# Kernel tuning notes

Hardware: AMD Instinct MI355X
Metric: run time of the kernel (lower is better)

Reference implementation:

```python
import jax, jax.numpy as jnp
import numpy as np

D_LATENT = 8
N_CENTERS = 48
CHANNELS = 64
PM_STEPS = 4
DT, BETA, CLAMP = 0.12, 1.0, 3.0
SIGMA_E, SIGMA_I, K_E, K_I, GAIN = 0.6, 1.2, 0.8, 1.0, 0.06


def setup_inputs() -> dict:
    key = jax.random.key(0)
    ks = jax.random.split(key, 12)
    B = 8192
    x = jax.random.normal(ks[0], (B, 784), dtype=jnp.float32)
    # encoder params (torch Linear default-ish init scale)
    W1 = jax.random.normal(ks[1], (784, 256), dtype=jnp.float32) * (1.0 / np.sqrt(784))
    b1 = jnp.zeros((256,), jnp.float32)
    W2 = jax.random.normal(ks[2], (256, D_LATENT), dtype=jnp.float32) * (1.0 / np.sqrt(256))
    b2 = jnp.zeros((D_LATENT,), jnp.float32)
    centers = jax.random.normal(ks[3], (N_CENTERS, D_LATENT), dtype=jnp.float32) * 0.7
    mus = jnp.ones((N_CENTERS,), jnp.float32) * 0.4
    projW = jax.random.normal(ks[4], (D_LATENT, CHANNELS), dtype=jnp.float32) * (1.0 / np.sqrt(D_LATENT))
    projb = jnp.zeros((CHANNELS,), jnp.float32)
    roW = jax.random.normal(ks[5], (CHANNELS, 10), dtype=jnp.float32) * (1.0 / np.sqrt(CHANNELS))
    rob = jnp.zeros((10,), jnp.float32)
    return {"x": x, "W1": W1, "b1": b1, "W2": W2, "b2": b2,
            "centers": centers, "mus": mus, "projW": projW, "projb": projb,
            "roW": roW, "rob": rob, "T": 5}


def _pm_field(z, centers, mus):
    # one PMField forward: `PM_STEPS` gradient-flow steps on z [B, d]
    for _ in range(PM_STEPS):
        diff = z[:, None, :] - centers[None, :, :]            # [B, C, d]
        r2 = jnp.sum(diff * diff, axis=-1) + 1e-4              # [B, C]
        r = jnp.sqrt(r2)
        n = 1.0 + jnp.sum(mus[None, :] / r, axis=1)            # [B]
        g = -jnp.sum(mus[None, :, None] * diff / (r * r2)[:, :, None], axis=1)  # [B, d]
        z = z + DT * BETA * (g / n[:, None])
        z = jnp.clip(z, -CLAMP, CLAMP)
    return z


def _lateral_ei(z, h):
    # kernel computed with no_grad in torch -> stop_gradient here
    sq = jnp.sum(z * z, axis=1)                                # [B]
    dist2 = jnp.maximum(sq[:, None] + sq[None, :] - 2.0 * (z @ z.T), 0.0)
    Ke = K_E * jnp.exp(-dist2 / (2.0 * SIGMA_E ** 2))
    Ki = K_I * jnp.exp(-dist2 / (2.0 * SIGMA_I ** 2))
    K = Ke - Ki
    K = K / (jnp.sum(K, axis=1, keepdims=True) + 1e-6)
    K = jax.lax.stop_gradient(K)
    return GAIN * (K @ h)


def reference(x, W1, b1, W2, b2, centers, mus, projW, projb, roW, rob, T):
    z = jnp.tanh(x @ W1 + b1) @ W2 + b2                        # encoder -> [B, d]
    h = jnp.zeros((x.shape[0], CHANNELS), x.dtype)
    logits = None
    for _ in range(T):
        z = _pm_field(z, centers, mus)
        h = 0.9 * h + 0.1 * jnp.tanh(z @ projW + projb)
        h = h + _lateral_ei(z, h)
        logits = h @ roW + rob
    return logits, z, h
```

## Files before the change

kernel.cpp:

```cpp
#include <hip/hip_runtime.h>
#include <hip/hip_bf16.h>
#include <math.h>

#define B_N      8192
#define IN_DIM   784
#define HID      256
#define DL       8
#define NC       48
#define CH       64
#define NCLS     10
#define T_ITERS  5
#define TILES    128

#define DT_      0.12f
#define CLAMP_   3.0f
#define GAIN_    0.06f
#define SQIL2    0.70776814f
#define ONE_BF16 0x3F80u

#if defined(__has_builtin)
#if __has_builtin(__builtin_amdgcn_exp2f)
#define EXP2(x) __builtin_amdgcn_exp2f(x)
#endif
#endif
#ifndef EXP2
#define EXP2(x) exp2f(x)
#endif

typedef __attribute__((ext_vector_type(8))) short short8v;
typedef __attribute__((ext_vector_type(4))) float f32x4;

__device__ __forceinline__ unsigned int pack_bf16_rhu(float lo, float hi) {
    unsigned int b0 = __builtin_bit_cast(unsigned int, lo);
    unsigned int b1 = __builtin_bit_cast(unsigned int, hi);
    return ((b0 + 0x8000u) >> 16) | ((b1 + 0x8000u) & 0xFFFF0000u);
}
__device__ __forceinline__ unsigned short bf16_1(float x) {
    return (unsigned short)((__builtin_bit_cast(unsigned int, x) + 0x8000u) >> 16);
}
__device__ __forceinline__ float bf16_to_f(unsigned short h) {
    return __builtin_bit_cast(float, ((unsigned int)h) << 16);
}

__device__ __forceinline__ void z_split(const float4 a, const float4 b,
                                        uint4& Whi, uint4& Wlo, unsigned int& Wc)
{
    float u[8] = {SQIL2*a.x, SQIL2*a.y, SQIL2*a.z, SQIL2*a.w,
                  SQIL2*b.x, SQIL2*b.y, SQIL2*b.z, SQIL2*b.w};
    float sq = 0.f;
    #pragma unroll
    for (int d = 0; d < 8; ++d) sq = fmaf(u[d], u[d], sq);
    float cn = -0.5f * sq;
    unsigned short hi[8]; float lo[8];
    #pragma unroll
    for (int d = 0; d < 8; ++d) {
        hi[d] = bf16_1(u[d]);
        lo[d] = u[d] - bf16_to_f(hi[d]);
    }
    unsigned short ch_ = bf16_1(cn);
    unsigned short cl_ = bf16_1(cn - bf16_to_f(ch_));
    Whi.x = (unsigned int)hi[0] | ((unsigned int)hi[1] << 16);
    Whi.y = (unsigned int)hi[2] | ((unsigned int)hi[3] << 16);
    Whi.z = (unsigned int)hi[4] | ((unsigned int)hi[5] << 16);
    Whi.w = (unsigned int)hi[6] | ((unsigned int)hi[7] << 16);
    Wlo.x = pack_bf16_rhu(lo[0], lo[1]); Wlo.y = pack_bf16_rhu(lo[2], lo[3]);
    Wlo.z = pack_bf16_rhu(lo[4], lo[5]); Wlo.w = pack_bf16_rhu(lo[6], lo[7]);
    Wc = (unsigned int)ch_ | ((unsigned int)cl_ << 16);
}

__global__ __launch_bounds__(256) void k_gemm1_tanh(
    const float* __restrict__ x, const float* __restrict__ W1,
    const float* __restrict__ b1, float* __restrict__ H1)
{
    __shared__ float As[16][36];
    __shared__ float Bs[16][64];
    const int tid = threadIdx.x;
    const int row0 = blockIdx.x * 32;
    const int col0 = blockIdx.y * 64;
    const int tr = tid >> 4, tc = tid & 15;
    float acc[2][4] = {};
    for (int k0 = 0; k0 < IN_DIM; k0 += 16) {
        if (tid < 128) {
            int m = tid >> 2, kq = tid & 3;
            float4 v = *(const float4*)(x + (size_t)(row0 + m) * IN_DIM + k0 + kq * 4);
            As[kq*4+0][m] = v.x; As[kq*4+1][m] = v.y;
            As[kq*4+2][m] = v.z; As[kq*4+3][m] = v.w;
        }
        {
            int kk = tid >> 4, n4 = tid & 15;
            *(float4*)(&Bs[kk][n4*4]) =
                *(const float4*)(W1 + (size_t)(k0 + kk) * HID + col0 + n4 * 4);
        }
        __syncthreads();
        #pragma unroll
        for (int kk = 0; kk < 16; ++kk) {
            float a0 = As[kk][tr*2];
            float a1 = As[kk][tr*2+1];
            float4 b = *(const float4*)(&Bs[kk][tc*4]);
            acc[0][0] += a0*b.x; acc[0][1] += a0*b.y;
            acc[0][2] += a0*b.z; acc[0][3] += a0*b.w;
            acc[1][0] += a1*b.x; acc[1][1] += a1*b.y;
            acc[1][2] += a1*b.z; acc[1][3] += a1*b.w;
        }
        __syncthreads();
    }
    #pragma unroll
    for (int i = 0; i < 2; ++i) {
        int r = row0 + tr*2 + i;
        #pragma unroll
        for (int j = 0; j < 4; ++j) {
            int c = col0 + tc*4 + j;
            H1[(size_t)r * HID + c] = tanhf(acc[i][j] + b1[c]);
        }
    }
}

__global__ __launch_bounds__(256) void k_gemm2(
    const float* __restrict__ H1, const float* __restrict__ W2,
    const float* __restrict__ b2, float* __restrict__ zbuf)
{
    __shared__ float W2s[HID][DL];
    const int tid = threadIdx.x;
    for (int l = tid; l < HID * DL; l += 256) W2s[l >> 3][l & 7] = W2[l];
    __syncthreads();
    const int row = blockIdx.x * 32 + (tid >> 3);
    const int d = tid & 7;
    float acc = b2[d];
    const float* hr = H1 + (size_t)row * HID;
    for (int k = 0; k < HID; k += 4) {
        float4 hv = *(const float4*)(hr + k);
        acc += hv.x * W2s[k][d] + hv.y * W2s[k+1][d]
             + hv.z * W2s[k+2][d] + hv.w * W2s[k+3][d];
    }
    zbuf[(size_t)row * DL + d] = acc;
}

template<int S, bool HP>
__global__ __launch_bounds__(256) void k_pm_proj(
    const float* __restrict__ centers, const float* __restrict__ mus,
    const float* __restrict__ projW, const float* __restrict__ projb,
    float* __restrict__ zbuf, float* __restrict__ hB,
    unsigned short* __restrict__ hTb,
    const float* __restrict__ pAcc, const float* __restrict__ pDen)
{
    __shared__ float4 cs4[NC][2];
    __shared__ float mu_s[NC];
    __shared__ float pW[DL][CH];
    __shared__ float pb[CH];
    const int tid = threadIdx.x;
    for (int l = tid; l < NC * 2; l += 256) cs4[l >> 1][l & 1] = ((const float4*)centers)[l];
    if (tid < NC) mu_s[tid] = mus[tid];
    for (int l = tid; l < DL * CH; l += 256) pW[l >> 6][l & 63] = projW[l];
    if (tid < CH) pb[tid] = projb[tid];
    __syncthreads();

    const int rloc = tid >> 3;
    const int dl = tid & 7;
    const int row = blockIdx.x * 32 + rloc;

    float4 cza[6], czb[6];
    float mur[6];
    #pragma unroll
    for (int k = 0; k < 6; ++k) {
        cza[k] = cs4[dl + 8*k][0];
        czb[k] = cs4[dl + 8*k][1];
        mur[k] = mu_s[dl + 8*k];
    }

    float z[8];
    {
        const float4* zp = (const float4*)(zbuf + (size_t)row * DL);
        float4 a = zp[0], b = zp[1];
        z[0]=a.x; z[1]=a.y; z[2]=a.z; z[3]=a.w;
        z[4]=b.x; z[5]=b.y; z[6]=b.z; z[7]=b.w;
    }

    #pragma unroll
    for (int step = 0; step < 4; ++step) {
        float np = 0.f;
        float gp[8] = {0,0,0,0,0,0,0,0};
        #pragma unroll
        for (int k = 0; k < 6; ++k) {
            float d0 = z[0]-cza[k].x, d1 = z[1]-cza[k].y;
            float d2 = z[2]-cza[k].z, d3 = z[3]-cza[k].w;
            float d4 = z[4]-czb[k].x, d5 = z[5]-czb[k].y;
            float d6 = z[6]-czb[k].z, d7 = z[7]-czb[k].w;
            float r2 = 1e-4f;
            r2 = fmaf(d0,d0,r2); r2 = fmaf(d1,d1,r2);
            r2 = fmaf(d2,d2,r2); r2 = fmaf(d3,d3,r2);
            r2 = fmaf(d4,d4,r2); r2 = fmaf(d5,d5,r2);
            r2 = fmaf(d6,d6,r2); r2 = fmaf(d7,d7,r2);
            float r = sqrtf(r2);
            float mr = mur[k] / r;
            np += mr;
            float t = mr / r2;
            gp[0] = fmaf(-t, d0, gp[0]); gp[1] = fmaf(-t, d1, gp[1]);
            gp[2] = fmaf(-t, d2, gp[2]); gp[3] = fmaf(-t, d3, gp[3]);
            gp[4] = fmaf(-t, d4, gp[4]); gp[5] = fmaf(-t, d5, gp[5]);
            gp[6] = fmaf(-t, d6, gp[6]); gp[7] = fmaf(-t, d7, gp[7]);
        }
        #pragma unroll
        for (int m = 1; m < 8; m <<= 1) {
            np += __shfl_xor(np, m);
            #pragma unroll
            for (int d = 0; d < 8; ++d) gp[d] += __shfl_xor(gp[d], m);
        }
        float s = DT_ / (1.f + np);
        #pragma unroll
        for (int d = 0; d < 8; ++d) {
            z[d] = fmaf(s, gp[d], z[d]);
            z[d] = fminf(fmaxf(z[d], -CLAMP_), CLAMP_);
        }
    }

    {
        float zout = z[0];
        #pragma unroll
        for (int d = 1; d < 8; ++d) zout = (dl == d) ? z[d] : zout;
        zbuf[(size_t)row * DL + dl] = zout;
    }

    const int c0 = dl * 8;
    float hin[8];
    if (HP) {
        float den = 1e-6f;
        #pragma unroll
        for (int s = 0; s < S; ++s) den += pDen[s * B_N + row];
        float inv = GAIN_ / den;
        #pragma unroll
        for (int q = 0; q < 2; ++q) {
            float4 a = {0.f, 0.f, 0.f, 0.f};
            #pragma unroll
            for (int s = 0; s < S; ++s) {
                float4 p = *(const float4*)(pAcc + (size_t)s * B_N * CH
                                            + (size_t)row * CH + c0 + q * 4);
                a.x += p.x; a.y += p.y; a.z += p.z; a.w += p.w;
            }
            float4 hm = *(const float4*)(hB + (size_t)row * CH + c0 + q * 4);
            hin[q*4+0] = fmaf(inv, a.x, hm.x);
            hin[q*4+1] = fmaf(inv, a.y, hm.y);
            hin[q*4+2] = fmaf(inv, a.z, hm.z);
            hin[q*4+3] = fmaf(inv, a.w, hm.w);
        }
    } else {
        #pragma unroll
        for (int k = 0; k < 8; ++k) hin[k] = 0.f;
    }
    #pragma unroll
    for (int k = 0; k < 8; ++k) {
        int c = c0 + k;
        float s = pb[c];
        #pragma unroll
        for (int dd = 0; dd < DL; ++dd) s = fmaf(z[dd], pW[dd][c], s);
        hin[k] = 0.9f * hin[k] + 0.1f * tanhf(s);
    }
    float4 o0 = {hin[0], hin[1], hin[2], hin[3]};
    float4 o1 = {hin[4], hin[5], hin[6], hin[7]};
    *(float4*)(hB + (size_t)row * CH + c0)     = o0;
    *(float4*)(hB + (size_t)row * CH + c0 + 4) = o1;

    {
        const int jl = row & 63;
        const int colp = (jl & 35) | ((jl & 12) << 1) | ((jl & 16) >> 2);
        const size_t tb = (size_t)(row & ~63) + colp;
        #pragma unroll
        for (int k = 0; k < 8; ++k)
            hTb[(size_t)(c0 + k) * B_N + tb] = bf16_1(hin[k]);
    }
}

template<int S>
__global__ __launch_bounds__(128, 2) void k_lateral(
    const float* __restrict__ zbuf, const unsigned short* __restrict__ hTb,
    float* __restrict__ pAcc, float* __restrict__ pDen)
{
    __shared__ __align__(16) unsigned short zA[2][64 * 24];
    __shared__ __align__(16) unsigned short hsT[2][CH][72];
    const int tid  = threadIdx.x;
    const int lane = tid & 63;
    const int wv   = tid >> 6;
    const int l15  = lane & 15;
    const int g    = lane >> 4;
    const int rowbase = blockIdx.x * 64;
    const int t0 = (TILES * blockIdx.y) / S;
    const int t1 = (TILES * (blockIdx.y + 1)) / S;
    const int chS = tid >> 1, hfS = tid & 1;

    short8v bZa, bZb;
    #pragma unroll
    for (int setb = 0; setb < 2; ++setb) {
        const int irow = rowbase + 32 * wv + 16 * setb + l15;
        const float4* zp = (const float4*)(zbuf + (size_t)irow * DL);
        uint4 Whi, Wlo; unsigned int Wc;
        z_split(zp[0], zp[1], Whi, Wlo, Wc);
        union { unsigned int u[4]; short8v v; } uh, ul, ua;
        uh.u[0]=Whi.x; uh.u[1]=Whi.y; uh.u[2]=Whi.z; uh.u[3]=Whi.w;
        ul.u[0]=Wlo.x; ul.u[1]=Wlo.y; ul.u[2]=Wlo.z; ul.u[3]=Wlo.w;
        ua.u[0] = ONE_BF16 | (ONE_BF16 << 16);
        ua.u[1] = Wc; ua.u[2] = 0; ua.u[3] = 0;
        short8v bz = (g == 2) ? ul.v : ((g == 3) ? ua.v : uh.v);
        if (setb == 0) bZa = bz; else bZb = bz;
    }
    const int offsh = (g == 1) ? 8 : ((g == 3) ? 16 : 0);

    short8v bones;
    {
        union { unsigned int u[4]; short8v v; } uo;
        uo.u[0] = uo.u[1] = uo.u[2] = uo.u[3] = ONE_BF16 | (ONE_BF16 << 16);
        bones = uo.v;
    }

    f32x4 accA0 = {0,0,0,0}, accA1 = {0,0,0,0}, accA2 = {0,0,0,0}, accA3 = {0,0,0,0};
    f32x4 accB0 = {0,0,0,0}, accB1 = {0,0,0,0}, accB2 = {0,0,0,0}, accB3 = {0,0,0,0};
    f32x4 acc4A = {0,0,0,0}, acc4B = {0,0,0,0};
    const f32x4 zc = {0,0,0,0};

    {
        const int jb = t0 * 64;
        if (tid < 64) {
            const float4* zp = (const float4*)(zbuf + (size_t)(jb + tid) * DL);
            uint4 Whi, Wlo; unsigned int Wc;
            z_split(zp[0], zp[1], Whi, Wlo, Wc);
            uint4 W2v; W2v.x = Wc; W2v.y = ONE_BF16 | (ONE_BF16 << 16);
            W2v.z = 0; W2v.w = 0;
            unsigned short* dst = &zA[0][tid * 24];
            *(uint4*)(dst)      = Whi;
            *(uint4*)(dst + 8)  = Wlo;
            *(uint4*)(dst + 16) = W2v;
        }
        const unsigned short* hs = hTb + (size_t)chS * B_N + jb + hfS * 32;
        *(uint4*)(&hsT[0][chS][hfS*32])      = *(const uint4*)(hs);
        *(uint4*)(&hsT[0][chS][hfS*32 + 8])  = *(const uint4*)(hs + 8);
        *(uint4*)(&hsT[0][chS][hfS*32 + 16]) = *(const uint4*)(hs + 16);
        *(uint4*)(&hsT[0][chS][hfS*32 + 24]) = *(const uint4*)(hs + 24);
    }

    #pragma unroll 1
    for (int jt = t0; jt < t1; ++jt) {
        const int cur = (jt - t0) & 1;
        const bool more = (jt + 1 < t1);
        uint4 h0n, h1n, h2n, h3n;
        float4 zna, znb;
        if (more) {
            const int jb2 = (jt + 1) * 64;
            const unsigned short* hs = hTb + (size_t)chS * B_N + jb2 + hfS * 32;
            h0n = *(const uint4*)(hs);
            h1n = *(const uint4*)(hs + 8);
            h2n = *(const uint4*)(hs + 16);
            h3n = *(const uint4*)(hs + 24);
            if (tid < 64) {
                const float4* zp = (const float4*)(zbuf + (size_t)(jb2 + tid) * DL);
                zna = zp[0]; znb = zp[1];
            }
        }
        __syncthreads();

        f32x4 gacA[4], gacB[4];
        #pragma unroll
        for (int t = 0; t < 4; ++t) {
            short8v az = *(const short8v*)(&zA[cur][(t * 16 + l15) * 24 + offsh]);
            gacA[t] = __builtin_amdgcn_mfma_f32_16x16x32_bf16(az, bZa, zc, 0, 0, 0);
            gacB[t] = __builtin_amdgcn_mfma_f32_16x16x32_bf16(az, bZb, zc, 0, 0, 0);
        }

        short8v afrA[2], afrB[2];
        #pragma unroll
        for (int kb = 0; kb < 2; ++kb) {
            float w8[8];
            #pragma unroll
            for (int m = 0; m < 8; ++m) {
                float out = gacA[2 * kb + (m >> 2)][m & 3];
                float e1 = EXP2(out);
                float e2 = e1 * e1;
                float e4 = e2 * e2;
                float e8 = e4 * e4;
                w8[m] = fmaf(0.8f, e8, -e2);
            }
            union { unsigned int u[4]; short8v v; } uf;
            uf.u[0] = pack_bf16_rhu(w8[0], w8[1]);
            uf.u[1] = pack_bf16_rhu(w8[2], w8[3]);
            uf.u[2] = pack_bf16_rhu(w8[4], w8[5]);
            uf.u[3] = pack_bf16_rhu(w8[6], w8[7]);
            afrA[kb] = uf.v;
        }
        #pragma unroll
        for (int kb = 0; kb < 2; ++kb) {
            float w8[8];
            #pragma unroll
            for (int m = 0; m < 8; ++m) {
                float out = gacB[2 * kb + (m >> 2)][m & 3];
                float e1 = EXP2(out);
                float e2 = e1 * e1;
                float e4 = e2 * e2;
                float e8 = e4 * e4;
                w8[m] = fmaf(0.8f, e8, -e2);
            }
            union { unsigned int u[4]; short8v v; } uf;
            uf.u[0] = pack_bf16_rhu(w8[0], w8[1]);
            uf.u[1] = pack_bf16_rhu(w8[2], w8[3]);
            uf.u[2] = pack_bf16_rhu(w8[4], w8[5]);
            uf.u[3] = pack_bf16_rhu(w8[6], w8[7]);
            afrB[kb] = uf.v;
        }

        #pragma unroll
        for (int kb = 0; kb < 2; ++kb) {
            const int jo = kb * 32 + g * 8;
            short8v b0 = *(const short8v*)&hsT[cur][ 0 + l15][jo];
            short8v b1 = *(const short8v*)&hsT[cur][16 + l15][jo];
            short8v b2 = *(const short8v*)&hsT[cur][32 + l15][jo];
            short8v b3 = *(const short8v*)&hsT[cur][48 + l15][jo];
            accA0 = __builtin_amdgcn_mfma_f32_16x16x32_bf16(afrA[kb], b0, accA0, 0, 0, 0);
            accA1 = __builtin_amdgcn_mfma_f32_16x16x32_bf16(afrA[kb], b1, accA1, 0, 0, 0);
            accA2 = __builtin_amdgcn_mfma_f32_16x16x32_bf16(afrA[kb], b2, accA2, 0, 0, 0);
            accA3 = __builtin_amdgcn_mfma_f32_16x16x32_bf16(afrA[kb], b3, accA3, 0, 0, 0);
            accB0 = __builtin_amdgcn_mfma_f32_16x16x32_bf16(afrB[kb], b0, accB0, 0, 0, 0);
            accB1 = __builtin_amdgcn_mfma_f32_16x16x32_bf16(afrB[kb], b1, accB1, 0, 0, 0);
            accB2 = __builtin_amdgcn_mfma_f32_16x16x32_bf16(afrB[kb], b2, accB2, 0, 0, 0);
            accB3 = __builtin_amdgcn_mfma_f32_16x16x32_bf16(afrB[kb], b3, accB3, 0, 0, 0);
            acc4A = __builtin_amdgcn_mfma_f32_16x16x32_bf16(afrA[kb], bones, acc4A, 0, 0, 0);
            acc4B = __builtin_amdgcn_mfma_f32_16x16x32_bf16(afrB[kb], bones, acc4B, 0, 0, 0);
        }
        __syncthreads();

        if (more) {
            const int nb = cur ^ 1;
            if (tid < 64) {
                uint4 Whi, Wlo; unsigned int Wc;
                z_split(zna, znb, Whi, Wlo, Wc);
                uint4 W2v; W2v.x = Wc; W2v.y = ONE_BF16 | (ONE_BF16 << 16);
                W2v.z = 0; W2v.w = 0;
                unsigned short* dst = &zA[nb][tid * 24];
                *(uint4*)(dst)      = Whi;
                *(uint4*)(dst + 8)  = Wlo;
                *(uint4*)(dst + 16) = W2v;
            }
            *(uint4*)(&hsT[nb][chS][hfS*32])      = h0n;
            *(uint4*)(&hsT[nb][chS][hfS*32 + 8])  = h1n;
            *(uint4*)(&hsT[nb][chS][hfS*32 + 16]) = h2n;
            *(uint4*)(&hsT[nb][chS][hfS*32 + 24]) = h3n;
        }
    }

    float* pA = pAcc + (size_t)blockIdx.y * (B_N * CH) + (size_t)rowbase * CH;
    #pragma unroll
    for (int r = 0; r < 4; ++r) {
        int giA = 32 * wv + g * 4 + r;
        int giB = giA + 16;
        pA[(size_t)giA * CH +  0 + l15] = accA0[r];
        pA[(size_t)giA * CH + 16 + l15] = accA1[r];
        pA[(size_t)giA * CH + 32 + l15] = accA2[r];
        pA[(size_t)giA * CH + 48 + l15] = accA3[r];
        pA[(size_t)giB * CH +  0 + l15] = accB0[r];
        pA[(size_t)giB * CH + 16 + l15] = accB1[r];
        pA[(size_t)giB * CH + 32 + l15] = accB2[r];
        pA[(size_t)giB * CH + 48 + l15] = accB3[r];
    }
    if (l15 == 0) {
        #pragma unroll
        for (int r = 0; r < 4; ++r) {
            pDen[blockIdx.y * B_N + rowbase + 32 * wv + g * 4 + r]      = acc4A[r];
            pDen[blockIdx.y * B_N + rowbase + 32 * wv + 16 + g * 4 + r] = acc4B[r];
        }
    }
}

template<int S>
__global__ __launch_bounds__(256) void k_logits_h(
    const float* __restrict__ hmid, const float* __restrict__ pAcc,
    const float* __restrict__ pDen, const float* __restrict__ roW,
    const float* __restrict__ rob, float* __restrict__ out_logits,
    float* __restrict__ out_h)
{
    __shared__ float hsh[64][68];
    __shared__ float ro[CH][NCLS];
    __shared__ float rb[NCLS];
    const int tid = threadIdx.x;
    for (int l = tid; l < CH * NCLS; l += 256) ro[l / NCLS][l % NCLS] = roW[l];
    if (tid < NCLS) rb[tid] = rob[tid];
    const int rowbase = blockIdx.x * 64;
    const int r  = tid >> 2;
    const int c0 = (tid & 3) * 16;
    const int row = rowbase + r;
    float den = 1e-6f;
    #pragma unroll
    for (int s = 0; s < S; ++s) den += pDen[s * B_N + row];
    float inv = GAIN_ / den;
    #pragma unroll
    for (int q = 0; q < 4; ++q) {
        float4 a = {0.f, 0.f, 0.f, 0.f};
        #pragma unroll
        for (int s = 0; s < S; ++s) {
            float4 p = *(const float4*)(pAcc + (size_t)s * B_N * CH
                                        + (size_t)row * CH + c0 + q * 4);
            a.x += p.x; a.y += p.y; a.z += p.z; a.w += p.w;
        }
        float4 hm = *(const float4*)(hmid + (size_t)row * CH + c0 + q * 4);
        float4 hv;
        hv.x = fmaf(inv, a.x, hm.x); hv.y = fmaf(inv, a.y, hm.y);
        hv.z = fmaf(inv, a.z, hm.z); hv.w = fmaf(inv, a.w, hm.w);
        *(float4*)(&hsh[r][c0 + q * 4]) = hv;
        *(float4*)(out_h + (size_t)row * CH + c0 + q * 4) = hv;
    }
    __syncthreads();
    for (int idx = tid; idx < 64 * NCLS; idx += 256) {
        int rr = idx / NCLS, o = idx % NCLS;
        float s = rb[o];
        #pragma unroll
        for (int k = 0; k < CH; ++k) s = fmaf(hsh[rr][k], ro[k][o], s);
        out_logits[(size_t)(rowbase + rr) * NCLS + o] = s;
    }
}

template<int S>
static void run_all(const float* x, const float* W1, const float* b1,
                    const float* W2, const float* b2, const float* centers,
                    const float* mus, const float* projW, const float* projb,
                    const float* roW, const float* rob,
                    float* ws, float* out, hipStream_t stream)
{
    float* pAcc = ws;
    float* pDen = ws + (size_t)S * B_N * CH;
    float* zbuf = pDen + (size_t)S * B_N;
    float* hB   = zbuf + B_N * DL;
    unsigned short* hTb = (unsigned short*)(hB + B_N * CH);
    float* H1   = ws;

    float* out_logits = out;
    float* out_z      = out + 81920;
    float* out_h      = out_z + 65536;

    k_gemm1_tanh<<<dim3(B_N / 32, HID / 64), 256, 0, stream>>>(x, W1, b1, H1);
    k_gemm2<<<B_N / 32, 256, 0, stream>>>(H1, W2, b2, zbuf);

    for (int t = 0; t < T_ITERS; ++t) {
        if (t == 0)
            k_pm_proj<S, false><<<B_N / 32, 256, 0, stream>>>(
                centers, mus, projW, projb, zbuf, hB, hTb, pAcc, pDen);
        else
            k_pm_proj<S, true><<<B_N / 32, 256, 0, stream>>>(
                centers, mus, projW, projb, zbuf, hB, hTb, pAcc, pDen);
        k_lateral<S><<<dim3(TILES, S), 128, 0, stream>>>(zbuf, hTb, pAcc, pDen);
    }

    k_logits_h<S><<<TILES, 256, 0, stream>>>(hB, pAcc, pDen, roW, rob,
                                             out_logits, out_h);
    hipMemcpyAsync(out_z, zbuf, (size_t)B_N * DL * sizeof(float),
                   hipMemcpyDeviceToDevice, stream);
}

extern "C" void kernel_launch(void* const* d_in, const int* in_sizes, int n_in,
                              void* d_out, int out_size, void* d_ws, size_t ws_size,
                              hipStream_t stream)
{
    const float* x       = (const float*)d_in[0];
    const float* W1      = (const float*)d_in[1];
    const float* b1      = (const float*)d_in[2];
    const float* W2      = (const float*)d_in[3];
    const float* b2      = (const float*)d_in[4];
    const float* centers = (const float*)d_in[5];
    const float* mus     = (const float*)d_in[6];
    const float* projW   = (const float*)d_in[7];
    const float* projb   = (const float*)d_in[8];
    const float* roW     = (const float*)d_in[9];
    const float* rob     = (const float*)d_in[10];

    float* ws  = (float*)d_ws;
    float* out = (float*)d_out;

    const size_t needS8 = ((size_t)8*B_N*CH + 8*B_N + B_N*DL + B_N*CH + B_N*CH/2) * 4;
    const size_t needS4 = ((size_t)4*B_N*CH + 4*B_N + B_N*DL + B_N*CH + B_N*CH/2) * 4;

    if (ws_size >= needS8)
        run_all<8>(x, W1, b1, W2, b2, centers, mus, projW, projb, roW, rob, ws, out, stream);
    else if (ws_size >= needS4)
        run_all<4>(x, W1, b1, W2, b2, centers, mus, projW, projb, roW, rob, ws, out, stream);
    else
        run_all<2>(x, W1, b1, W2, b2, centers, mus, projW, projb, roW, rob, ws, out, stream);
}
```

Measured before the change: 328.8 us.

## Retile encoder GEMM to 64x64 double-buffered tiles; trim lateral-kernel sync

The first encoder GEMM now uses 64-row tiles with a 4x4 per-thread microtile. Next-k-slice loads are prefetched into registers while the current shared-memory buffer is consumed, which needs only one barrier per k-step. Bias is loaded as float4 and output is written as float4. In the lateral kernel, MFMA sections are wrapped in s_setprio, and the barrier after the accumulation MFMAs is removed, relying on double-buffering plus the top-of-loop barrier. This aims to cut GEMM load/sync overhead and lateral-loop stalls, at the cost of more registers in the GEMM.

```diff
diff --git a/kernel.cpp b/kernel.cpp
--- a/kernel.cpp
+++ b/kernel.cpp
@@ -72,46 +72,67 @@
     const float* __restrict__ x, const float* __restrict__ W1,
     const float* __restrict__ b1, float* __restrict__ H1)
 {
-    __shared__ float As[16][36];
-    __shared__ float Bs[16][64];
+    __shared__ float As[2][16][68];
+    __shared__ float Bs[2][16][64];
     const int tid = threadIdx.x;
-    const int row0 = blockIdx.x * 32;
+    const int row0 = blockIdx.x * 64;
     const int col0 = blockIdx.y * 64;
     const int tr = tid >> 4, tc = tid & 15;
-    float acc[2][4] = {};
-    for (int k0 = 0; k0 < IN_DIM; k0 += 16) {
-        if (tid < 128) {
-            int m = tid >> 2, kq = tid & 3;
-            float4 v = *(const float4*)(x + (size_t)(row0 + m) * IN_DIM + k0 + kq * 4);
-            As[kq*4+0][m] = v.x; As[kq*4+1][m] = v.y;
-            As[kq*4+2][m] = v.z; As[kq*4+3][m] = v.w;
-        }
-        {
-            int kk = tid >> 4, n4 = tid & 15;
-            *(float4*)(&Bs[kk][n4*4]) =
-                *(const float4*)(W1 + (size_t)(k0 + kk) * HID + col0 + n4 * 4);
+    const int am = tid >> 2, akq = tid & 3;
+    const int bkk = tid >> 4, bn4 = tid & 15;
+    float acc[4][4] = {};
+
+    {
+        float4 va = *(const float4*)(x + (size_t)(row0 + am) * IN_DIM + akq * 4);
+        float4 vb = *(const float4*)(W1 + (size_t)bkk * HID + col0 + bn4 * 4);
+        As[0][akq*4+0][am] = va.x; As[0][akq*4+1][am] = va.y;
+        As[0][akq*4+2][am] = va.z; As[0][akq*4+3][am] = va.w;
+        *(float4*)(&Bs[0][bkk][bn4*4]) = vb;
+    }
+
+    const int NK = IN_DIM / 16;
+    #pragma unroll 1
+    for (int ks = 0; ks < NK; ++ks) {
+        const int cur = ks & 1;
+        const bool more = (ks + 1 < NK);
+        float4 va, vb;
+        if (more) {
+            const int k0 = (ks + 1) * 16;
+            va = *(const float4*)(x + (size_t)(row0 + am) * IN_DIM + k0 + akq * 4);
+            vb = *(const float4*)(W1 + (size_t)(k0 + bkk) * HID + col0 + bn4 * 4);
         }
         __syncthreads();
         #pragma unroll
         for (int kk = 0; kk < 16; ++kk) {
-            float a0 = As[kk][tr*2];
-            float a1 = As[kk][tr*2+1];
-            float4 b = *(const float4*)(&Bs[kk][tc*4]);
-            acc[0][0] += a0*b.x; acc[0][1] += a0*b.y;
-            acc[0][2] += a0*b.z; acc[0][3] += a0*b.w;
-            acc[1][0] += a1*b.x; acc[1][1] += a1*b.y;
-            acc[1][2] += a1*b.z; acc[1][3] += a1*b.w;
-        }
-        __syncthreads();
-    }
-    #pragma unroll
-    for (int i = 0; i < 2; ++i) {
-        int r = row0 + tr*2 + i;
-        #pragma unroll
-        for (int j = 0; j < 4; ++j) {
-            int c = col0 + tc*4 + j;
-            H1[(size_t)r * HID + c] = tanhf(acc[i][j] + b1[c]);
-        }
+            float4 a = *(const float4*)(&As[cur][kk][tr*4]);
+            float4 b = *(const float4*)(&Bs[cur][kk][tc*4]);
+            float av[4] = {a.x, a.y, a.z, a.w};
+            float bv[4] = {b.x, b.y, b.z, b.w};
+            #pragma unroll
+            for (int i = 0; i < 4; ++i)
+                #pragma unroll
+                for (int j = 0; j < 4; ++j)
+                    acc[i][j] += av[i] * bv[j];
+        }
+        if (more) {
+            const int nb = cur ^ 1;
+            As[nb][akq*4+0][am] = va.x; As[nb][akq*4+1][am] = va.y;
+            As[nb][akq*4+2][am] = va.z; As[nb][akq*4+3][am] = va.w;
+            *(float4*)(&Bs[nb][bkk][bn4*4]) = vb;
+        }
+    }
+
+    const float4 b1c = *(const float4*)(b1 + col0 + tc * 4);
+    const float bb[4] = {b1c.x, b1c.y, b1c.z, b1c.w};
+    #pragma unroll
+    for (int i = 0; i < 4; ++i) {
+        int r = row0 + tr*4 + i;
+        float4 hv;
+        hv.x = tanhf(acc[i][0] + bb[0]);
+        hv.y = tanhf(acc[i][1] + bb[1]);
+        hv.z = tanhf(acc[i][2] + bb[2]);
+        hv.w = tanhf(acc[i][3] + bb[3]);
+        *(float4*)(H1 + (size_t)r * HID + col0 + tc * 4) = hv;
     }
 }
 
@@ -356,12 +377,14 @@
         __syncthreads();
 
         f32x4 gacA[4], gacB[4];
+        __builtin_amdgcn_s_setprio(1);
         #pragma unroll
         for (int t = 0; t < 4; ++t) {
             short8v az = *(const short8v*)(&zA[cur][(t * 16 + l15) * 24 + offsh]);
             gacA[t] = __builtin_amdgcn_mfma_f32_16x16x32_bf16(az, bZa, zc, 0, 0, 0);
             gacB[t] = __builtin_amdgcn_mfma_f32_16x16x32_bf16(az, bZb, zc, 0, 0, 0);
         }
+        __builtin_amdgcn_s_setprio(0);
 
         short8v afrA[2], afrB[2];
         #pragma unroll
@@ -403,6 +426,7 @@
             afrB[kb] = uf.v;
         }
 
+        __builtin_amdgcn_s_setprio(1);
         #pragma unroll
         for (int kb = 0; kb < 2; ++kb) {
             const int jo = kb * 32 + g * 8;
@@ -421,7 +445,7 @@
             acc4A = __builtin_amdgcn_mfma_f32_16x16x32_bf16(afrA[kb], bones, acc4A, 0, 0, 0);
             acc4B = __builtin_amdgcn_mfma_f32_16x16x32_bf16(afrB[kb], bones, acc4B, 0, 0, 0);
         }
-        __syncthreads();
+        __builtin_amdgcn_s_setprio(0);
 
         if (more) {
             const int nb = cur ^ 1;
@@ -530,7 +554,7 @@
     float* out_z      = out + 81920;
     float* out_h      = out_z + 65536;
 
-    k_gemm1_tanh<<<dim3(B_N / 32, HID / 64), 256, 0, stream>>>(x, W1, b1, H1);
+    k_gemm1_tanh<<<dim3(B_N / 64, HID / 64), 256, 0, stream>>>(x, W1, b1, H1);
     k_gemm2<<<B_N / 32, 256, 0, stream>>>(H1, W2, b2, zbuf);
 
     for (int t = 0; t < T_ITERS; ++t) {
```

Measured after the change: 307.0 us. 6.6% less time.
